# Performance work log

Measured on AMD Instinct MI355X. Metric: run time of the kernel, lower is better.

## Reference

```python
import jax, jax.numpy as jnp
import numpy as np


def shift_2d(x, H, W):
    # x: (B, T=H*W, C); quarter-channel directional shifts (gamma=1/4), C must be divisible by 4
    B, T, C = x.shape
    g = C // 4
    xi = x.reshape(B, H, W, C)
    # group 0: shift right along W (output[..., 1:, :] = input[..., :-1, :])
    s0 = jnp.pad(xi[:, :, : W - 1, 0:g], ((0, 0), (0, 0), (1, 0), (0, 0)))
    # group 1: shift left along W
    s1 = jnp.pad(xi[:, :, 1:, g : 2 * g], ((0, 0), (0, 0), (0, 1), (0, 0)))
    # group 2: shift down along H
    s2 = jnp.pad(xi[:, : H - 1, :, 2 * g : 3 * g], ((0, 0), (1, 0), (0, 0), (0, 0)))
    # group 3: shift up along H
    s3 = jnp.pad(xi[:, 1:, :, 3 * g : 4 * g], ((0, 0), (0, 1), (0, 0), (0, 0)))
    out = jnp.concatenate([s0, s1, s2, s3], axis=-1)  # C == 4*g here
    return out.reshape(B, T, C)


def wkv(w, u, k, v):
    # RWKV v4 WKV recurrence with running-max numerical stabilization.
    # w, u: (C,) ; k, v: (B, T, C) ; returns y: (B, T, C)
    B, T, C = k.shape
    NEG = jnp.float32(-1e38)

    def step(carry, kv):
        p, q, o = carry  # numerator state, denominator state, running log-max
        kt, vt = kv
        no = jnp.maximum(o, u + kt)
        A = jnp.exp(o - no)
        Bc = jnp.exp(u + kt - no)
        y = (A * p + Bc * vt) / (A * q + Bc)
        no2 = jnp.maximum(w + o, kt)
        A2 = jnp.exp(w + o - no2)
        B2 = jnp.exp(kt - no2)
        return (A2 * p + B2 * vt, A2 * q + B2, no2), y

    init = (jnp.zeros((B, C), k.dtype), jnp.zeros((B, C), k.dtype), jnp.full((B, C), NEG, k.dtype))
    kT = jnp.moveaxis(k, 1, 0)
    vT = jnp.moveaxis(v, 1, 0)
    _, yT = jax.lax.scan(step, init, (kT, vT))
    return jnp.moveaxis(yT, 0, 1)


def setup_inputs() -> dict:
    key = jax.random.key(0)
    ks = jax.random.split(key, 7)
    B, H, W, C = 16, 96, 96, 192
    T = H * W
    x = jax.random.normal(ks[0], (B, T, C), jnp.float32)
    Wk = jax.random.normal(ks[1], (C, C), jnp.float32) * 0.02
    Wv = jax.random.normal(ks[2], (C, C), jnp.float32) * 0.02
    Wr = jax.random.normal(ks[3], (C, C), jnp.float32) * 0.02
    Wo = jax.random.normal(ks[4], (C, C), jnp.float32) * 0.02
    spatial_decay = jax.random.normal(ks[5], (3, C), jnp.float32)
    spatial_first = jax.random.normal(ks[6], (3, C), jnp.float32)
    return {"x": x, "Wk": Wk, "Wv": Wv, "Wr": Wr, "Wo": Wo,
            "spatial_decay": spatial_decay, "spatial_first": spatial_first,
            "H": H, "W": W}


def reference(x, Wk, Wv, Wr, Wo, spatial_decay, spatial_first, H, W):
    B, T, C = x.shape
    xs = shift_2d(x, H, W)
    k = xs @ Wk.T
    v = xs @ Wv.T
    sr = jax.nn.sigmoid(xs @ Wr.T)
    w = spatial_decay[0] / T
    u = spatial_first[0] / T
    y = wkv(w, u, k, v)
    return (sr * y) @ Wo.T
```

## Files before the change

### kernel.cpp

```cpp
#include <hip/hip_runtime.h>
#include <hip/hip_bf16.h>

typedef __bf16 bf16x8 __attribute__((ext_vector_type(8)));
typedef float f32x4 __attribute__((ext_vector_type(4)));

using bf = __hip_bfloat16;

constexpr int cB = 16, cH = 96, cW = 96, cC = 192;
constexpr int cT = cH * cW;
constexpr int cM = cB * cT;
constexpr int CH = 48;
constexpr int NS = cT / CH;
constexpr int NTM = cM / 64;
constexpr float Tinv = 1.0f / 9216.0f;

__device__ __forceinline__ int swz(int row, int bytecol) {
    return row * 384 + (bytecol ^ ((row & 7) << 4));
}
__device__ __forceinline__ float bflo(unsigned u) { return __uint_as_float(u << 16); }
__device__ __forceinline__ float bfhi(unsigned u) { return __uint_as_float(u & 0xffff0000u); }

__global__ __launch_bounds__(256) void convw_k(
    const float* __restrict__ Wk, const float* __restrict__ Wv,
    const float* __restrict__ Wr, const float* __restrict__ Wo,
    bf* __restrict__ out)
{
    int i = (blockIdx.x * 256 + threadIdx.x) * 8;
    int mat = i / 36864, off = i % 36864;
    const float* s = mat == 0 ? Wk : (mat == 1 ? Wv : (mat == 2 ? Wr : Wo));
    const float4* sp = reinterpret_cast<const float4*>(s + off);
    float4 a0 = sp[0], a1 = sp[1];
    bf16x8 pk;
    pk[0]=(__bf16)a0.x; pk[1]=(__bf16)a0.y; pk[2]=(__bf16)a0.z; pk[3]=(__bf16)a0.w;
    pk[4]=(__bf16)a1.x; pk[5]=(__bf16)a1.y; pk[6]=(__bf16)a1.z; pk[7]=(__bf16)a1.w;
    *reinterpret_cast<bf16x8*>(reinterpret_cast<__bf16*>(out) + i) = pk;
}

__global__ __launch_bounds__(768) void gemm0f(
    const float* __restrict__ Ap, const bf* __restrict__ Wb,
    bf* __restrict__ O0, bf* __restrict__ O1, bf* __restrict__ O2)
{
    __shared__ char lds[64 * 384];
    char* Ab = &lds[0];
    const int tid = threadIdx.x, bx = blockIdx.x;
    const int lane = tid & 63, wid = tid >> 6;
    const int mat = wid >> 2, strip = wid & 3;
    const int lr = lane & 15, lq = lane >> 4;

    bf16x8 bw[3][6];
    {
        const bf* Wt = Wb + (size_t)mat * 192 * cC;
#pragma unroll
        for (int nt = 0; nt < 3; ++nt)
#pragma unroll
            for (int kk = 0; kk < 6; ++kk)
                bw[nt][kk] = *reinterpret_cast<const bf16x8*>(
                    Wt + (size_t)(strip * 48 + nt * 16 + lr) * cC + kk * 32 + lq * 8);
    }

    int rj[2], kbj[2];
#pragma unroll
    for (int j = 0; j < 2; ++j) { int idx = tid + j * 768; rj[j] = idx / 24; kbj[j] = idx % 24; }

    bf* Os = (mat == 0 ? O0 : (mat == 1 ? O1 : O2));

    for (int i = 0; i < 9; ++i) {
        const int tix = bx + 256 * i;
#pragma unroll
        for (int j = 0; j < 2; ++j) {
            int gm = tix * 64 + rj[j];
            int b = gm / cT, t = gm % cT, h = t / cW, w = t % cW;
            int grp = kbj[j] / 6;
            int hs = h + (grp == 2 ? -1 : (grp == 3 ? 1 : 0));
            int ws2 = w + (grp == 0 ? -1 : (grp == 1 ? 1 : 0));
            float4 a0{0,0,0,0}, a1{0,0,0,0};
            if (hs >= 0 && hs < cH && ws2 >= 0 && ws2 < cW) {
                const float4* s = reinterpret_cast<const float4*>(
                    Ap + ((size_t)b * cT + (size_t)hs * cW + ws2) * cC + kbj[j] * 8);
                a0 = s[0]; a1 = s[1];
            }
            bf16x8 pk;
            pk[0]=(__bf16)a0.x; pk[1]=(__bf16)a0.y; pk[2]=(__bf16)a0.z; pk[3]=(__bf16)a0.w;
            pk[4]=(__bf16)a1.x; pk[5]=(__bf16)a1.y; pk[6]=(__bf16)a1.z; pk[7]=(__bf16)a1.w;
            *reinterpret_cast<bf16x8*>(Ab + swz(rj[j], kbj[j] * 16)) = pk;
        }
        __syncthreads();

#pragma unroll
        for (int mh = 0; mh < 2; ++mh) {
            f32x4 acc[2][3] = {};
#pragma unroll
            for (int kk = 0; kk < 6; ++kk) {
                const int bc = kk * 64 + lq * 16;
                bf16x8 af[2];
#pragma unroll
                for (int mt = 0; mt < 2; ++mt)
                    af[mt] = *reinterpret_cast<const bf16x8*>(
                        Ab + swz(mh * 32 + mt * 16 + lr, bc));
#pragma unroll
                for (int mt = 0; mt < 2; ++mt)
#pragma unroll
                    for (int nt = 0; nt < 3; ++nt)
                        acc[mt][nt] = __builtin_amdgcn_mfma_f32_16x16x32_bf16(
                            af[mt], bw[nt][kk], acc[mt][nt], 0, 0, 0);
            }
#pragma unroll
            for (int mt = 0; mt < 2; ++mt)
#pragma unroll
                for (int nt = 0; nt < 3; ++nt)
#pragma unroll
                    for (int j = 0; j < 4; ++j) {
                        int row = tix * 64 + mh * 32 + mt * 16 + lq * 4 + j;
                        int col = strip * 48 + nt * 16 + lr;
                        float v = acc[mt][nt][j];
                        if (mat == 2) v = 1.0f / (1.0f + __expf(-v));
                        Os[(size_t)row * cC + col] = __float2bfloat16(v);
                    }
        }
        __syncthreads();
    }
}

__global__ __launch_bounds__(512, 4) void gemm1f(
    const bf* __restrict__ Az, const bf* __restrict__ Wb,
    float* __restrict__ Out)
{
    __shared__ char lds[64 * 384];
    char* Ab = &lds[0];
    const int tid = threadIdx.x, bx = blockIdx.x;
    const int lane = tid & 63, wid = tid >> 6;
    const int wm = wid >> 2, wn = wid & 3;
    const int lr = lane & 15, lq = lane >> 4;

    bf16x8 bw[3][6];
#pragma unroll
    for (int nt = 0; nt < 3; ++nt)
#pragma unroll
        for (int kk = 0; kk < 6; ++kk)
            bw[nt][kk] = *reinterpret_cast<const bf16x8*>(
                Wb + (size_t)(wn * 48 + nt * 16 + lr) * cC + kk * 32 + lq * 8);

    int rj[3], kbj[3];
#pragma unroll
    for (int j = 0; j < 3; ++j) { int idx = tid + j * 512; rj[j] = idx / 24; kbj[j] = idx % 24; }

    for (int tix = bx; tix < NTM; tix += 512) {
#pragma unroll
        for (int j = 0; j < 3; ++j) {
            int4 val = *reinterpret_cast<const int4*>(
                Az + (size_t)(tix * 64 + rj[j]) * cC + kbj[j] * 8);
            *reinterpret_cast<int4*>(Ab + swz(rj[j], kbj[j] * 16)) = val;
        }
        __syncthreads();
#pragma unroll
        for (int mh = 0; mh < 2; ++mh) {
            f32x4 acc[3] = {};
#pragma unroll
            for (int kk = 0; kk < 6; ++kk) {
                const int bc = kk * 64 + lq * 16;
                bf16x8 af = *reinterpret_cast<const bf16x8*>(
                    Ab + swz(wm * 32 + mh * 16 + lr, bc));
#pragma unroll
                for (int nt = 0; nt < 3; ++nt)
                    acc[nt] = __builtin_amdgcn_mfma_f32_16x16x32_bf16(
                        af, bw[nt][kk], acc[nt], 0, 0, 0);
            }
#pragma unroll
            for (int nt = 0; nt < 3; ++nt)
#pragma unroll
                for (int j = 0; j < 4; ++j) {
                    int row = tix * 64 + wm * 32 + mh * 16 + lq * 4 + j;
                    int col = wn * 48 + nt * 16 + lr;
                    Out[(size_t)row * cC + col] = acc[nt][j];
                }
        }
        __syncthreads();
    }
}

__global__ __launch_bounds__(192) void wkv_pass1(
    const bf* __restrict__ k, const bf* __restrict__ v,
    const float* __restrict__ sd,
    float* __restrict__ stP, float* __restrict__ stQ, float* __restrict__ stO)
{
    const int c2 = threadIdx.x % 96, sub = threadIdx.x / 96;
    const int b = blockIdx.y, ch = blockIdx.x * 2 + sub;
    const int c0 = c2 * 2;
    const float w0 = sd[c0] * Tinv, w1 = sd[c0 + 1] * Tinv;
    size_t base = ((size_t)b * cT + (size_t)ch * CH) * cC + c0;
    float p0 = 0.f, q0 = 0.f, o0 = -1e38f;
    float p1 = 0.f, q1 = 0.f, o1 = -1e38f;
    unsigned kwc = *reinterpret_cast<const unsigned*>(k + base);
    unsigned vwc = *reinterpret_cast<const unsigned*>(v + base);
    for (int s = 0; s < CH; ++s) {
        unsigned kwn = 0, vwn = 0;
        if (s + 1 < CH) {
            kwn = *reinterpret_cast<const unsigned*>(k + base + (size_t)(s + 1) * cC);
            vwn = *reinterpret_cast<const unsigned*>(v + base + (size_t)(s + 1) * cC);
        }
        float kt0 = bflo(kwc), kt1 = bfhi(kwc);
        float vt0 = bflo(vwc), vt1 = bfhi(vwc);
        float no0 = fmaxf(w0 + o0, kt0);
        float A0 = __expf(w0 + o0 - no0), B0 = __expf(kt0 - no0);
        p0 = A0 * p0 + B0 * vt0; q0 = A0 * q0 + B0; o0 = no0;
        float no1 = fmaxf(w1 + o1, kt1);
        float A1 = __expf(w1 + o1 - no1), B1 = __expf(kt1 - no1);
        p1 = A1 * p1 + B1 * vt1; q1 = A1 * q1 + B1; o1 = no1;
        kwc = kwn; vwc = vwn;
    }
    size_t si = ((size_t)b * NS + ch) * cC + c0;
    *reinterpret_cast<float2*>(stP + si) = make_float2(p0, p1);
    *reinterpret_cast<float2*>(stQ + si) = make_float2(q0, q1);
    *reinterpret_cast<float2*>(stO + si) = make_float2(o0, o1);
}

__global__ __launch_bounds__(192) void wkv_pass2(
    float* __restrict__ stP, float* __restrict__ stQ, float* __restrict__ stO,
    const float* __restrict__ sd)
{
    const int c = threadIdx.x, b = blockIdx.x;
    const float w = sd[c] * Tinv;
    const float Lw = w * (float)CH;
    float p = 0.f, q = 0.f, o = -1e38f;
    size_t si = (size_t)b * NS * cC + c;
    float sp = stP[si], sq = stQ[si], so = stO[si];
    for (int ch = 0; ch < NS; ++ch) {
        float np_ = 0.f, nq_ = 0.f, no_ = -1e38f;
        if (ch + 1 < NS) {
            size_t sj = si + (size_t)(ch + 1) * cC;
            np_ = stP[sj]; nq_ = stQ[sj]; no_ = stO[sj];
        }
        size_t sc = si + (size_t)ch * cC;
        stP[sc] = p; stQ[sc] = q; stO[sc] = o;
        float po = o + Lw;
        float m = fmaxf(po, so);
        float e1 = __expf(po - m), e2 = __expf(so - m);
        p = e1 * p + e2 * sp;
        q = e1 * q + e2 * sq;
        o = m;
        sp = np_; sq = nq_; so = no_;
    }
}

__global__ __launch_bounds__(192) void wkv_pass3(
    const bf* __restrict__ k, const bf* __restrict__ v, const bf* __restrict__ sr,
    const float* __restrict__ sd, const float* __restrict__ sf,
    const float* __restrict__ iP, const float* __restrict__ iQ,
    const float* __restrict__ iO, bf* __restrict__ z)
{
    const int c2 = threadIdx.x % 96, sub = threadIdx.x / 96;
    const int b = blockIdx.y, ch = blockIdx.x * 2 + sub;
    const int c0 = c2 * 2;
    const float w0 = sd[c0] * Tinv, w1 = sd[c0 + 1] * Tinv;
    const float u0 = sf[c0] * Tinv, u1 = sf[c0 + 1] * Tinv;
    size_t si = ((size_t)b * NS + ch) * cC + c0;
    float2 pp = *reinterpret_cast<const float2*>(iP + si);
    float2 qq = *reinterpret_cast<const float2*>(iQ + si);
    float2 oo = *reinterpret_cast<const float2*>(iO + si);
    float p0 = pp.x, q0 = qq.x, o0 = oo.x;
    float p1 = pp.y, q1 = qq.y, o1 = oo.y;
    size_t base = ((size_t)b * cT + (size_t)ch * CH) * cC + c0;
    unsigned kwc = *reinterpret_cast<const unsigned*>(k + base);
    unsigned vwc = *reinterpret_cast<const unsigned*>(v + base);
    unsigned rwc = *reinterpret_cast<const unsigned*>(sr + base);
    for (int s = 0; s < CH; ++s) {
        unsigned kwn = 0, vwn = 0, rwn = 0;
        if (s + 1 < CH) {
            size_t nx = base + (size_t)(s + 1) * cC;
            kwn = *reinterpret_cast<const unsigned*>(k + nx);
            vwn = *reinterpret_cast<const unsigned*>(v + nx);
            rwn = *reinterpret_cast<const unsigned*>(sr + nx);
        }
        float kt0 = bflo(kwc), kt1 = bfhi(kwc);
        float vt0 = bflo(vwc), vt1 = bfhi(vwc);
        float rt0 = bflo(rwc), rt1 = bfhi(rwc);

        float no0 = fmaxf(o0, u0 + kt0);
        float Ae0 = __expf(o0 - no0), Be0 = __expf(u0 + kt0 - no0);
        float y0 = (Ae0 * p0 + Be0 * vt0) / (Ae0 * q0 + Be0);
        float no1 = fmaxf(o1, u1 + kt1);
        float Ae1 = __expf(o1 - no1), Be1 = __expf(u1 + kt1 - no1);
        float y1 = (Ae1 * p1 + Be1 * vt1) / (Ae1 * q1 + Be1);

        bf z0 = __float2bfloat16(rt0 * y0);
        bf z1 = __float2bfloat16(rt1 * y1);
        unsigned zp = (unsigned)*reinterpret_cast<unsigned short*>(&z0)
                    | ((unsigned)*reinterpret_cast<unsigned short*>(&z1) << 16);
        *reinterpret_cast<unsigned*>(z + base + (size_t)s * cC) = zp;

        float m0 = fmaxf(w0 + o0, kt0);
        float A0 = __expf(w0 + o0 - m0), B0 = __expf(kt0 - m0);
        p0 = A0 * p0 + B0 * vt0; q0 = A0 * q0 + B0; o0 = m0;
        float m1 = fmaxf(w1 + o1, kt1);
        float A1 = __expf(w1 + o1 - m1), B1 = __expf(kt1 - m1);
        p1 = A1 * p1 + B1 * vt1; q1 = A1 * q1 + B1; o1 = m1;
        kwc = kwn; vwc = vwn; rwc = rwn;
    }
}

extern "C" void kernel_launch(void* const* d_in, const int* in_sizes, int n_in,
                              void* d_out, int out_size, void* d_ws, size_t ws_size,
                              hipStream_t stream)
{
    const float* x  = (const float*)d_in[0];
    const float* Wk = (const float*)d_in[1];
    const float* Wv = (const float*)d_in[2];
    const float* Wr = (const float*)d_in[3];
    const float* Wo = (const float*)d_in[4];
    const float* sd = (const float*)d_in[5];
    const float* sf = (const float*)d_in[6];
    float* out = (float*)d_out;

    const size_t nEl = (size_t)cM * cC;
    bf* kbuf  = (bf*)d_out;
    bf* srbuf = (bf*)d_out + nEl;
    char* ws = (char*)d_ws;
    bf* vbuf = (bf*)ws;
    bf* zbuf = (bf*)(ws + 2 * nEl);
    const size_t stN = (size_t)cB * NS * cC;
    float* stP = (float*)(ws + 4 * nEl);
    float* stQ = stP + stN;
    float* stO = stQ + stN;
    bf* wbf = (bf*)(stO + stN);

    convw_k<<<dim3(72), dim3(256), 0, stream>>>(Wk, Wv, Wr, Wo, wbf);
    gemm0f<<<dim3(256), dim3(768), 0, stream>>>(x, wbf, kbuf, vbuf, srbuf);
    wkv_pass1<<<dim3(NS / 2, cB), dim3(192), 0, stream>>>(kbuf, vbuf, sd, stP, stQ, stO);
    wkv_pass2<<<dim3(cB), dim3(192), 0, stream>>>(stP, stQ, stO, sd);
    wkv_pass3<<<dim3(NS / 2, cB), dim3(192), 0, stream>>>(
        kbuf, vbuf, srbuf, sd, sf, stP, stQ, stO, zbuf);
    gemm1f<<<dim3(512), dim3(512), 0, stream>>>(
        zbuf, wbf + (size_t)576 * cC, out);
}
```

Measured before the change: 223.2 us.

## Double-buffer A tiles in both GEMM kernels via register prefetch

Both GEMM kernels now issue the global loads for the next A tile into registers before computing on the current tile. Those registers are then written into a second LDS buffer, which removes one barrier per iteration and hides global load latency behind the MFMA work. The cost is doubled shared memory per block and more live registers, which could lower occupancy. gemm0f also gains a min-blocks launch bound hint of 3.

Result: slower. 232.0 us (+4.0%).

```diff
diff --git a/kernel.cpp b/kernel.cpp
--- a/kernel.cpp
+++ b/kernel.cpp
@@ -36,12 +36,11 @@
     *reinterpret_cast<bf16x8*>(reinterpret_cast<__bf16*>(out) + i) = pk;
 }
 
-__global__ __launch_bounds__(768) void gemm0f(
+__global__ __launch_bounds__(768, 3) void gemm0f(
     const float* __restrict__ Ap, const bf* __restrict__ Wb,
     bf* __restrict__ O0, bf* __restrict__ O1, bf* __restrict__ O2)
 {
-    __shared__ char lds[64 * 384];
-    char* Ab = &lds[0];
+    __shared__ char lds[2 * 64 * 384];
     const int tid = threadIdx.x, bx = blockIdx.x;
     const int lane = tid & 63, wid = tid >> 6;
     const int mat = wid >> 2, strip = wid & 3;
@@ -62,30 +61,44 @@
 #pragma unroll
     for (int j = 0; j < 2; ++j) { int idx = tid + j * 768; rj[j] = idx / 24; kbj[j] = idx % 24; }
 
-    bf* Os = (mat == 0 ? O0 : (mat == 1 ? O1 : O2));
-
-    for (int i = 0; i < 9; ++i) {
-        const int tix = bx + 256 * i;
+    float4 pfA[4];
+
+    auto loadA = [&](int tile) {
 #pragma unroll
         for (int j = 0; j < 2; ++j) {
-            int gm = tix * 64 + rj[j];
+            int gm = tile * 64 + rj[j];
             int b = gm / cT, t = gm % cT, h = t / cW, w = t % cW;
             int grp = kbj[j] / 6;
             int hs = h + (grp == 2 ? -1 : (grp == 3 ? 1 : 0));
             int ws2 = w + (grp == 0 ? -1 : (grp == 1 ? 1 : 0));
-            float4 a0{0,0,0,0}, a1{0,0,0,0};
+            pfA[2*j] = float4{0,0,0,0}; pfA[2*j+1] = float4{0,0,0,0};
             if (hs >= 0 && hs < cH && ws2 >= 0 && ws2 < cW) {
                 const float4* s = reinterpret_cast<const float4*>(
                     Ap + ((size_t)b * cT + (size_t)hs * cW + ws2) * cC + kbj[j] * 8);
-                a0 = s[0]; a1 = s[1];
+                pfA[2*j] = s[0]; pfA[2*j+1] = s[1];
             }
+        }
+    };
+    auto writeA = [&](int bufIdx) {
+        char* An = &lds[0] + bufIdx * (64 * 384);
+#pragma unroll
+        for (int j = 0; j < 2; ++j) {
             bf16x8 pk;
-            pk[0]=(__bf16)a0.x; pk[1]=(__bf16)a0.y; pk[2]=(__bf16)a0.z; pk[3]=(__bf16)a0.w;
-            pk[4]=(__bf16)a1.x; pk[5]=(__bf16)a1.y; pk[6]=(__bf16)a1.z; pk[7]=(__bf16)a1.w;
-            *reinterpret_cast<bf16x8*>(Ab + swz(rj[j], kbj[j] * 16)) = pk;
-        }
-        __syncthreads();
-
+            pk[0]=(__bf16)pfA[2*j].x; pk[1]=(__bf16)pfA[2*j].y; pk[2]=(__bf16)pfA[2*j].z; pk[3]=(__bf16)pfA[2*j].w;
+            pk[4]=(__bf16)pfA[2*j+1].x; pk[5]=(__bf16)pfA[2*j+1].y; pk[6]=(__bf16)pfA[2*j+1].z; pk[7]=(__bf16)pfA[2*j+1].w;
+            *reinterpret_cast<bf16x8*>(An + swz(rj[j], kbj[j] * 16)) = pk;
+        }
+    };
+
+    bf* Os = (mat == 0 ? O0 : (mat == 1 ? O1 : O2));
+
+    loadA(bx); writeA(0);
+    __syncthreads();
+
+    for (int i = 0; i < 9; ++i) {
+        const int tix = bx + 256 * i;
+        if (i < 8) loadA(bx + 256 * (i + 1));
+        char* Ab = &lds[0] + (i & 1) * (64 * 384);
 #pragma unroll
         for (int mh = 0; mh < 2; ++mh) {
             f32x4 acc[2][3] = {};
@@ -117,6 +130,7 @@
                         Os[(size_t)row * cC + col] = __float2bfloat16(v);
                     }
         }
+        if (i < 8) writeA((i + 1) & 1);
         __syncthreads();
     }
 }
@@ -125,8 +139,7 @@
     const bf* __restrict__ Az, const bf* __restrict__ Wb,
     float* __restrict__ Out)
 {
-    __shared__ char lds[64 * 384];
-    char* Ab = &lds[0];
+    __shared__ char lds[2 * 64 * 384];
     const int tid = threadIdx.x, bx = blockIdx.x;
     const int lane = tid & 63, wid = tid >> 6;
     const int wm = wid >> 2, wn = wid & 3;
@@ -144,14 +157,27 @@
 #pragma unroll
     for (int j = 0; j < 3; ++j) { int idx = tid + j * 512; rj[j] = idx / 24; kbj[j] = idx % 24; }
 
-    for (int tix = bx; tix < NTM; tix += 512) {
-#pragma unroll
-        for (int j = 0; j < 3; ++j) {
-            int4 val = *reinterpret_cast<const int4*>(
-                Az + (size_t)(tix * 64 + rj[j]) * cC + kbj[j] * 8);
-            *reinterpret_cast<int4*>(Ab + swz(rj[j], kbj[j] * 16)) = val;
-        }
-        __syncthreads();
+    int4 piA[3];
+    auto loadA = [&](int tile) {
+#pragma unroll
+        for (int j = 0; j < 3; ++j)
+            piA[j] = *reinterpret_cast<const int4*>(
+                Az + (size_t)(tile * 64 + rj[j]) * cC + kbj[j] * 8);
+    };
+    auto writeA = [&](int bufIdx) {
+        char* An = &lds[0] + bufIdx * (64 * 384);
+#pragma unroll
+        for (int j = 0; j < 3; ++j)
+            *reinterpret_cast<int4*>(An + swz(rj[j], kbj[j] * 16)) = piA[j];
+    };
+
+    loadA(bx); writeA(0);
+    __syncthreads();
+
+    int step = 0;
+    for (int tix = bx; tix < NTM; tix += 512, ++step) {
+        if (tix + 512 < NTM) loadA(tix + 512);
+        char* Ab = &lds[0] + (step & 1) * (64 * 384);
 #pragma unroll
         for (int mh = 0; mh < 2; ++mh) {
             f32x4 acc[3] = {};
@@ -174,6 +200,7 @@
                     Out[(size_t)row * cC + col] = acc[nt][j];
                 }
         }
+        if (tix + 512 < NTM) writeA((step + 1) & 1);
         __syncthreads();
     }
 }
```
